# Kernel tuning notes

Hardware: AMD Instinct MI355X
Metric: run time of the kernel (lower is better)

## Reference

```python
import jax, jax.numpy as jnp
import numpy as np

B, S = 32, 2048
D = 128      # embedding_dim
H = 256      # hidden_dim
K = 512      # codebook_size
RECON_COEF, COMMIT_COEF, VQ_COEF = 1.0, 0.15, 0.05


def _conv1d(x, w, b):
    # x: [B, Cin, S], w: [Cout, Cin, 3], 'SAME' padding (padding=1, k=3)
    y = jax.lax.conv_general_dilated(x, w, window_strides=(1,), padding='SAME',
                                     dimension_numbers=('NCH', 'OIH', 'NCH'))
    return y + b[None, :, None]


def _lrelu(x):
    return jnp.where(x >= 0, x, 0.2 * x)


def setup_inputs() -> dict:
    key = jax.random.key(0)
    ks = jax.random.split(key, 14)

    def w(k, shape, fan_in):
        bound = 1.0 / np.sqrt(fan_in)
        return jax.random.uniform(k, shape, jnp.float32, -bound, bound)

    return {
        'x': jax.random.normal(ks[0], (B, S), jnp.float32),
        'codebook': jax.random.normal(ks[1], (K, D), jnp.float32),
        'ew1': w(ks[2], (H, 1, 3), 1 * 3),  'eb1': w(ks[3], (H,), 1 * 3),
        'ew2': w(ks[4], (H, H, 3), H * 3),  'eb2': w(ks[5], (H,), H * 3),
        'ew3': w(ks[6], (D, H, 3), H * 3),  'eb3': w(ks[7], (D,), H * 3),
        'dw1': w(ks[8], (H, D, 3), D * 3),  'db1': w(ks[9], (H,), D * 3),
        'dw2': w(ks[10], (H, H, 3), H * 3), 'db2': w(ks[11], (H,), H * 3),
        'dw3': w(ks[12], (1, H, 3), H * 3), 'db3': w(ks[13], (1,), H * 3),
    }


def reference(x, codebook, ew1, eb1, ew2, eb2, ew3, eb3, dw1, db1, dw2, db2, dw3, db3):
    # ---- encode ----
    h = x[:, None, :]                                  # [B,1,S]
    h = _lrelu(_conv1d(h, ew1, eb1))
    h = _lrelu(_conv1d(h, ew2, eb2))
    z = _conv1d(h, ew3, eb3)                           # [B,D,S]

    # ---- vector quantize (eval mode: no EMA update) ----
    zt = jnp.transpose(z, (0, 2, 1))                   # [B,S,D]
    z_flat = zt.reshape(-1, D)                         # [B*S,D]
    # squared distances: |z|^2 + |c|^2 - 2 z c^T
    d = (jnp.sum(z_flat ** 2, axis=1, keepdims=True)
         + jnp.sum(codebook ** 2, axis=1)
         - 2.0 * z_flat @ codebook.T)                  # [B*S,K]
    idx = jnp.argmin(d, axis=1)                        # [B*S]
    z_q = codebook[idx].reshape(zt.shape)              # [B,S,D] (== one-hot @ codebook)

    vq_loss = jnp.mean((jax.lax.stop_gradient(zt) - z_q) ** 2) * VQ_COEF
    commitment_loss = jnp.mean((zt - jax.lax.stop_gradient(z_q)) ** 2) * COMMIT_COEF
    indices = idx.reshape(B, S)

    # ---- decode ----
    h = jnp.transpose(z_q, (0, 2, 1))                  # [B,D,S]
    h = _lrelu(_conv1d(h, dw1, db1))
    h = _lrelu(_conv1d(h, dw2, db2))
    x_recon = _conv1d(h, dw3, db3)[:, 0, :]            # [B,S]

    recon_loss = jnp.mean((x - x_recon) ** 2) * RECON_COEF
    loss = recon_loss + vq_loss + commitment_loss
    return x_recon, indices, loss, recon_loss, vq_loss, commitment_loss
```

## Files before the change

kernel.cpp:

```cpp
#include <hip/hip_runtime.h>
#include <float.h>

#define S_LEN 2048
#define BATCH 32
#define HCH   256
#define DCH   128
#define KCODES 512

typedef float  f32x4  __attribute__((ext_vector_type(4)));
typedef short  bf16x8 __attribute__((ext_vector_type(8)));
typedef short  short8 __attribute__((ext_vector_type(8)));

__device__ __forceinline__ float lrelu_f(float v) { return v >= 0.f ? v : 0.2f * v; }

__device__ __forceinline__ short f2bf(float f) {
    unsigned u = __float_as_uint(f);
    u = u + 0x7fffu + ((u >> 16) & 1u);
    return (short)(u >> 16);
}
__device__ __forceinline__ float bf2f(unsigned short u) {
    return __uint_as_float(((unsigned)u) << 16);
}

__global__ void prep_cb_split_kernel(const float* __restrict__ cb,
                                     short* __restrict__ cb_hi, short* __restrict__ cb_lo,
                                     float* __restrict__ cnorm) {
    int k = blockIdx.x * 256 + threadIdx.x;
    if (k < KCODES) {
        float s = 0.f;
        for (int d = 0; d < DCH; ++d) {
            float v = cb[k * DCH + d];
            s += v * v;
            short hi = f2bf(v);
            short lo = f2bf(v - bf2f((unsigned short)hi));
            cb_hi[k * DCH + d] = hi;
            cb_lo[k * DCH + d] = lo;
        }
        cnorm[k] = s;
    }
}

__global__ void prep_w_split_kernel(const float* __restrict__ Wsrc,
                                    short* __restrict__ Wh, short* __restrict__ Wl,
                                    int Cout, int Cin) {
    int i = blockIdx.x * 256 + threadIdx.x;
    int total = 3 * Cout * Cin;
    if (i < total) {
        int t = i / (Cout * Cin);
        int rem = i - t * Cout * Cin;
        int co = rem / Cin;
        int ci = rem - co * Cin;
        float v = Wsrc[(co * Cin + ci) * 3 + t];
        short hi = f2bf(v);
        Wh[i] = hi;
        Wl[i] = f2bf(v - bf2f((unsigned short)hi));
    }
}

__global__ void prep_wdec_kernel(const float* __restrict__ Wsrc, short* __restrict__ Wdst,
                                 int Cin) {
    int i = blockIdx.x * 256 + threadIdx.x;
    int total = 3 * 256 * Cin;
    if (i < total) {
        int t = i / (256 * Cin);
        int rem = i - t * 256 * Cin;
        int co = rem / Cin;
        int ci = rem - co * Cin;
        Wdst[i] = f2bf(Wsrc[(co * Cin + ci) * 3 + t]);
    }
}

__global__ void prep_w3t_kernel(const float* __restrict__ w3, float* __restrict__ w3t) {
    int i = blockIdx.x * 256 + threadIdx.x;
    if (i < 768) {
        int t = i / 256, ci = i - t * 256;
        w3t[i] = w3[ci * 3 + t];
    }
}

__global__ __launch_bounds__(256) void enc_conv1_cl_kernel(
        const float* __restrict__ x, short* __restrict__ h_hi, short* __restrict__ h_lo,
        const float* __restrict__ w, const float* __restrict__ bias) {
    __shared__ float ws[HCH * 3];
    __shared__ float bs[HCH];
    int tid = threadIdx.x;
    for (int i = tid; i < HCH * 3; i += 256) ws[i] = w[i];
    for (int i = tid; i < HCH; i += 256) bs[i] = bias[i];
    __syncthreads();
    int b = blockIdx.y;
    int s = blockIdx.x * 32 + (tid >> 3);
    int cch = tid & 7;
    const float* xb = x + (size_t)b * S_LEN;
    float xm = (s > 0) ? xb[s - 1] : 0.f;
    float x0 = xb[s];
    float xp = (s < S_LEN - 1) ? xb[s + 1] : 0.f;
    size_t base = ((size_t)(b * S_LEN + s)) * HCH + cch * 32;
#pragma unroll
    for (int cc = 0; cc < 4; ++cc) {
        short8 oh, ol;
#pragma unroll
        for (int e = 0; e < 8; ++e) {
            int co = cch * 32 + cc * 8 + e;
            float v = ws[co * 3 + 0] * xm + ws[co * 3 + 1] * x0 + ws[co * 3 + 2] * xp + bs[co];
            v = lrelu_f(v);
            short hi = f2bf(v);
            oh[e] = hi;
            ol[e] = f2bf(v - bf2f((unsigned short)hi));
        }
        *(short8*)(h_hi + base + cc * 8) = oh;
        *(short8*)(h_lo + base + cc * 8) = ol;
    }
}

__global__ __launch_bounds__(256) void conv_mfma_split(
        const short* __restrict__ in_hi, const short* __restrict__ in_lo,
        short* __restrict__ out_hi, short* __restrict__ out_lo,
        const short* __restrict__ wt_hi, const short* __restrict__ wt_lo,
        const float* __restrict__ bias, int Cin, int Cout, int do_lrelu) {
    __shared__ short smem[17680];
    short* Xh = smem;
    short* Xl = smem + 130 * 68;

    const int tid = threadIdx.x;
    const int lane = tid & 63;
    const int w = tid >> 6;
    const int m = lane & 15;
    const int q = lane >> 4;
    const int sOff = (w & 1) * 64;
    const int cOff = (w >> 1) * 64;
    const int b = blockIdx.z;
    const int s0 = blockIdx.x * 128;
    const int co0 = blockIdx.y * 128;

    f32x4 acc[4][4];
    f32x4 zero4 = {0.f, 0.f, 0.f, 0.f};
#pragma unroll
    for (int i = 0; i < 4; ++i)
#pragma unroll
        for (int j = 0; j < 4; ++j) acc[i][j] = zero4;

    const short* inhb = in_hi + (size_t)b * S_LEN * Cin;
    const short* inlb = in_lo + (size_t)b * S_LEN * Cin;

    for (int ci0 = 0; ci0 < Cin; ci0 += 64) {
        __syncthreads();
        for (int c = tid; c < 2080; c += 256) {
            int r = c >> 4;
            int sub = c & 15;
            int half = sub >> 3;
            int part = sub & 7;
            int s = s0 - 1 + r;
            float4 v = make_float4(0.f, 0.f, 0.f, 0.f);
            if (s >= 0 && s < S_LEN) {
                size_t goff = (size_t)s * Cin + ci0 + part * 8;
                v = half ? *(const float4*)(inlb + goff) : *(const float4*)(inhb + goff);
            }
            *(float4*)((half ? Xl : Xh) + r * 68 + part * 8) = v;
        }
        __syncthreads();

#pragma unroll
        for (int ks = 0; ks < 2; ++ks) {
            const int kofs = ks * 32;
#pragma unroll
            for (int t = 0; t < 3; ++t) {
                bf16x8 ah[4], al[4], bh[4], bl[4];
#pragma unroll
                for (int j = 0; j < 4; ++j) {
                    size_t woff = ((size_t)(t * Cout + co0 + cOff + j * 16 + m)) * Cin + ci0 + kofs + q * 8;
                    bh[j] = *(const bf16x8*)(wt_hi + woff);
                    bl[j] = *(const bf16x8*)(wt_lo + woff);
                }
#pragma unroll
                for (int i = 0; i < 4; ++i) {
                    int row = sOff + i * 16 + m + t;
                    ah[i] = *(const bf16x8*)(Xh + row * 68 + kofs + q * 8);
                    al[i] = *(const bf16x8*)(Xl + row * 68 + kofs + q * 8);
                }
#pragma unroll
                for (int i = 0; i < 4; ++i)
#pragma unroll
                    for (int j = 0; j < 4; ++j) {
                        acc[i][j] = __builtin_amdgcn_mfma_f32_16x16x32_bf16(ah[i], bh[j], acc[i][j], 0, 0, 0);
                        acc[i][j] = __builtin_amdgcn_mfma_f32_16x16x32_bf16(ah[i], bl[j], acc[i][j], 0, 0, 0);
                        acc[i][j] = __builtin_amdgcn_mfma_f32_16x16x32_bf16(al[i], bh[j], acc[i][j], 0, 0, 0);
                    }
            }
        }
    }

    __syncthreads();
    short* obH = smem + w * 2560;
    short* obL = obH + 1280;
#pragma unroll
    for (int j = 0; j < 4; ++j) {
        float bv = bias[co0 + cOff + j * 16 + m];
#pragma unroll
        for (int i = 0; i < 4; ++i) {
#pragma unroll
            for (int r = 0; r < 4; ++r) {
                float val = acc[i][j][r] + bv;
                if (do_lrelu) val = lrelu_f(val);
                short hi = f2bf(val);
                short lo = f2bf(val - bf2f((unsigned short)hi));
                int row = i * 16 + q * 4 + r;
                obH[row * 20 + m] = hi;
                obL[row * 20 + m] = lo;
            }
        }
        const int colchunk = lane & 1;
        const int rbase = lane >> 1;
#pragma unroll
        for (int it = 0; it < 2; ++it) {
            int row = it * 32 + rbase;
            short8 vh = *(const short8*)(obH + row * 20 + colchunk * 8);
            short8 vl = *(const short8*)(obL + row * 20 + colchunk * 8);
            size_t goff = ((size_t)(b * S_LEN + s0 + sOff + row)) * Cout
                        + co0 + cOff + j * 16 + colchunk * 8;
            *(short8*)(out_hi + goff) = vh;
            *(short8*)(out_lo + goff) = vl;
        }
    }
}

__global__ __launch_bounds__(256) void vq_mfma_kernel(
        const short* __restrict__ z_hi, const short* __restrict__ z_lo,
        const short* __restrict__ cb_hi, const short* __restrict__ cb_lo,
        const float* __restrict__ cnorm, int* __restrict__ idx_out,
        float* __restrict__ idx_f_out) {
    __shared__ short smem[2 * 64 * 136];
    __shared__ float redv[64][4];
    __shared__ int   redi[64][4];
    short* Zh = smem;
    short* Zl = smem + 64 * 136;

    const int tid = threadIdx.x;
    const int lane = tid & 63;
    const int w = tid >> 6;
    const int m = lane & 15;
    const int q = lane >> 4;
    const int n0 = blockIdx.x * 64;

    for (int c = tid; c < 2048; c += 256) {
        int buf = c >> 10;
        int rem = c & 1023;
        int r = rem >> 4, part = rem & 15;
        size_t goff = (size_t)(n0 + r) * DCH + part * 8;
        float4 v = buf ? *(const float4*)(z_lo + goff) : *(const float4*)(z_hi + goff);
        *(float4*)((buf ? Zl : Zh) + r * 136 + part * 8) = v;
    }
    __syncthreads();

    float best[4][4];
    int besti[4][4];
#pragma unroll
    for (int i = 0; i < 4; ++i)
#pragma unroll
        for (int r = 0; r < 4; ++r) { best[i][r] = FLT_MAX; besti[i][r] = 0; }

    for (int k0 = 0; k0 < KCODES; k0 += 256) {
        f32x4 acc[4][4];
        f32x4 zero4 = {0.f, 0.f, 0.f, 0.f};
#pragma unroll
        for (int i = 0; i < 4; ++i)
#pragma unroll
            for (int j = 0; j < 4; ++j) acc[i][j] = zero4;

#pragma unroll
        for (int d0 = 0; d0 < DCH; d0 += 32) {
            bf16x8 ah[4], al[4], bh[4], bl[4];
#pragma unroll
            for (int j = 0; j < 4; ++j) {
                size_t coff = (size_t)(k0 + w * 64 + j * 16 + m) * DCH + d0 + q * 8;
                bh[j] = *(const bf16x8*)(cb_hi + coff);
                bl[j] = *(const bf16x8*)(cb_lo + coff);
            }
#pragma unroll
            for (int i = 0; i < 4; ++i) {
                int row = i * 16 + m;
                ah[i] = *(const bf16x8*)(Zh + row * 136 + d0 + q * 8);
                al[i] = *(const bf16x8*)(Zl + row * 136 + d0 + q * 8);
            }
#pragma unroll
            for (int i = 0; i < 4; ++i)
#pragma unroll
                for (int j = 0; j < 4; ++j) {
                    acc[i][j] = __builtin_amdgcn_mfma_f32_16x16x32_bf16(ah[i], bh[j], acc[i][j], 0, 0, 0);
                    acc[i][j] = __builtin_amdgcn_mfma_f32_16x16x32_bf16(ah[i], bl[j], acc[i][j], 0, 0, 0);
                    acc[i][j] = __builtin_amdgcn_mfma_f32_16x16x32_bf16(al[i], bh[j], acc[i][j], 0, 0, 0);
                }
        }
#pragma unroll
        for (int j = 0; j < 4; ++j) {
            int k = k0 + w * 64 + j * 16 + m;
            float cn = cnorm[k];
#pragma unroll
            for (int i = 0; i < 4; ++i)
#pragma unroll
                for (int r = 0; r < 4; ++r) {
                    float dv = cn - 2.f * acc[i][j][r];
                    if (dv < best[i][r]) { best[i][r] = dv; besti[i][r] = k; }
                }
        }
    }

#pragma unroll
    for (int mask = 1; mask < 16; mask <<= 1) {
#pragma unroll
        for (int i = 0; i < 4; ++i)
#pragma unroll
            for (int r = 0; r < 4; ++r) {
                float ov = __shfl_xor(best[i][r], mask);
                int oi = __shfl_xor(besti[i][r], mask);
                if (ov < best[i][r] || (ov == best[i][r] && oi < besti[i][r])) {
                    best[i][r] = ov; besti[i][r] = oi;
                }
            }
    }
    if (m == 0) {
#pragma unroll
        for (int i = 0; i < 4; ++i)
#pragma unroll
            for (int r = 0; r < 4; ++r) {
                int srow = i * 16 + q * 4 + r;
                redv[srow][w] = best[i][r];
                redi[srow][w] = besti[i][r];
            }
    }
    __syncthreads();
    if (tid < 64) {
        float bv = redv[tid][0];
        int bi = redi[tid][0];
#pragma unroll
        for (int w2 = 1; w2 < 4; ++w2) {
            float v = redv[tid][w2];
            int ii = redi[tid][w2];
            if (v < bv || (v == bv && ii < bi)) { bv = v; bi = ii; }
        }
        int n = n0 + tid;
        idx_out[n] = bi;
        idx_f_out[n] = (float)bi;
    }
}

__global__ __launch_bounds__(256) void gather_vqsum_kernel(
        const float* __restrict__ cb, const int* __restrict__ idxb,
        const short* __restrict__ z_hi, const short* __restrict__ z_lo,
        short* __restrict__ zq, float* __restrict__ acc_vq) {
    int tid = threadIdx.x;
    int b = blockIdx.y;
    int s = blockIdx.x * 32 + (tid >> 3);
    int dpart = tid & 7;
    int n = b * S_LEN + s;
    int k = idxb[n];
    const float* src = cb + (size_t)k * DCH + dpart * 16;
    size_t zoff = (size_t)n * DCH + dpart * 16;
    float sum = 0.f;
    short8 outv[2];
#pragma unroll
    for (int half = 0; half < 2; ++half) {
        float4 f0 = *(const float4*)(src + half * 8);
        float4 f1 = *(const float4*)(src + half * 8 + 4);
        bf16x8 zh = *(const bf16x8*)(z_hi + zoff + half * 8);
        bf16x8 zl = *(const bf16x8*)(z_lo + zoff + half * 8);
        float qv[8] = {f0.x, f0.y, f0.z, f0.w, f1.x, f1.y, f1.z, f1.w};
        short8 o;
#pragma unroll
        for (int e = 0; e < 8; ++e) {
            o[e] = f2bf(qv[e]);
            float zv = bf2f((unsigned short)zh[e]) + bf2f((unsigned short)zl[e]);
            float df = zv - qv[e];
            sum += df * df;
        }
        outv[half] = o;
    }
    *(short8*)(zq + zoff) = outv[0];
    *(short8*)(zq + zoff + 8) = outv[1];
    for (int off = 32; off > 0; off >>= 1) sum += __shfl_down(sum, off);
    __shared__ float wsum[4];
    if ((tid & 63) == 0) wsum[tid >> 6] = sum;
    __syncthreads();
    if (tid == 0) atomicAdd(acc_vq, wsum[0] + wsum[1] + wsum[2] + wsum[3]);
}

__global__ __launch_bounds__(256) void conv_mfma_cl(
        const short* __restrict__ in, short* __restrict__ out,
        const short* __restrict__ wt, const float* __restrict__ bias,
        int Cin) {
    __shared__ short smem[8840];
    short* Xs = smem;

    const int tid = threadIdx.x;
    const int lane = tid & 63;
    const int w = tid >> 6;
    const int m = lane & 15;
    const int q = lane >> 4;
    const int sOff = (w & 1) * 64;
    const int cOff = (w >> 1) * 64;
    const int b = blockIdx.z;
    const int s0 = blockIdx.x * 128;
    const int co0 = blockIdx.y * 128;

    f32x4 acc[4][4];
    f32x4 zero4 = {0.f, 0.f, 0.f, 0.f};
#pragma unroll
    for (int i = 0; i < 4; ++i)
#pragma unroll
        for (int j = 0; j < 4; ++j) acc[i][j] = zero4;

    const short* inb = in + (size_t)b * S_LEN * Cin;

    for (int ci0 = 0; ci0 < Cin; ci0 += 64) {
        __syncthreads();
        for (int c = tid; c < 1040; c += 256) {
            int r = c >> 3;
            int part = c & 7;
            int s = s0 - 1 + r;
            float4 v = make_float4(0.f, 0.f, 0.f, 0.f);
            if (s >= 0 && s < S_LEN)
                v = *(const float4*)(inb + (size_t)s * Cin + ci0 + part * 8);
            *(float4*)(Xs + r * 68 + part * 8) = v;
        }
        __syncthreads();

#pragma unroll
        for (int ks = 0; ks < 2; ++ks) {
            const int kofs = ks * 32;
#pragma unroll
            for (int t = 0; t < 3; ++t) {
                bf16x8 a[4], bb[4];
#pragma unroll
                for (int j = 0; j < 4; ++j)
                    bb[j] = *(const bf16x8*)(wt + ((size_t)(t * 256 + co0 + cOff + j * 16 + m)) * Cin + ci0 + kofs + q * 8);
#pragma unroll
                for (int i = 0; i < 4; ++i)
                    a[i] = *(const bf16x8*)(Xs + (sOff + i * 16 + m + t) * 68 + kofs + q * 8);
#pragma unroll
                for (int i = 0; i < 4; ++i)
#pragma unroll
                    for (int j = 0; j < 4; ++j)
                        acc[i][j] = __builtin_amdgcn_mfma_f32_16x16x32_bf16(
                            a[i], bb[j], acc[i][j], 0, 0, 0);
            }
        }
    }

    __syncthreads();
    short* ob = smem + w * 1280;
#pragma unroll
    for (int j = 0; j < 4; ++j) {
        float bv = bias[co0 + cOff + j * 16 + m];
#pragma unroll
        for (int i = 0; i < 4; ++i) {
#pragma unroll
            for (int r = 0; r < 4; ++r) {
                float val = acc[i][j][r] + bv;
                val = lrelu_f(val);
                ob[(i * 16 + q * 4 + r) * 20 + m] = f2bf(val);
            }
        }
        const int colchunk = lane & 1;
        const int rbase = lane >> 1;
#pragma unroll
        for (int it = 0; it < 2; ++it) {
            int row = it * 32 + rbase;
            short8 v = *(const short8*)(ob + row * 20 + colchunk * 8);
            size_t goff = ((size_t)(b * S_LEN + s0 + sOff + row)) * 256
                        + co0 + cOff + j * 16 + colchunk * 8;
            *(short8*)(out + goff) = v;
        }
    }
}

__global__ __launch_bounds__(256) void dec_conv3_tiled_kernel(
        const short* __restrict__ h, const float* __restrict__ w3t,
        const float* __restrict__ b3, const float* __restrict__ x,
        float* __restrict__ xr, float* __restrict__ acc_recon) {
    __shared__ short Zs[66 * 264];
    __shared__ float ws[3 * 256];
    __shared__ float wsum[4];
    int tid = threadIdx.x;
    int b = blockIdx.y;
    int s0 = blockIdx.x * 64;
    const short* hb = h + (size_t)b * S_LEN * HCH;
    for (int i = tid; i < 768; i += 256) ws[i] = w3t[i];
    for (int c = tid; c < 2112; c += 256) {
        int r = c >> 5, part = c & 31;
        int g = s0 - 1 + r;
        short8 v = {0, 0, 0, 0, 0, 0, 0, 0};
        if (g >= 0 && g < S_LEN)
            v = *(const short8*)(hb + (size_t)g * HCH + part * 8);
        *(short8*)(Zs + r * 264 + part * 8) = v;
    }
    __syncthreads();

    int quarter = tid & 3;
    int sl = tid >> 2;
    float a0 = 0.f, a1 = 0.f, a2 = 0.f, a3 = 0.f;
#pragma unroll
    for (int t = 0; t < 3; ++t) {
        const short* zrow = Zs + (sl + t) * 264 + quarter * 64;
        const float* wrow = ws + t * 256 + quarter * 64;
#pragma unroll
        for (int c = 0; c < 8; ++c) {
            bf16x8 v = *(const bf16x8*)(zrow + c * 8);
            float4 w0 = *(const float4*)(wrow + c * 8);
            float4 w1 = *(const float4*)(wrow + c * 8 + 4);
            a0 = fmaf(w0.x, bf2f((unsigned short)v[0]), a0);
            a1 = fmaf(w0.y, bf2f((unsigned short)v[1]), a1);
            a2 = fmaf(w0.z, bf2f((unsigned short)v[2]), a2);
            a3 = fmaf(w0.w, bf2f((unsigned short)v[3]), a3);
            a0 = fmaf(w1.x, bf2f((unsigned short)v[4]), a0);
            a1 = fmaf(w1.y, bf2f((unsigned short)v[5]), a1);
            a2 = fmaf(w1.z, bf2f((unsigned short)v[6]), a2);
            a3 = fmaf(w1.w, bf2f((unsigned short)v[7]), a3);
        }
    }
    float acc = (a0 + a1) + (a2 + a3);
    acc += __shfl_xor(acc, 1);
    acc += __shfl_xor(acc, 2);
    float df2 = 0.f;
    if (quarter == 0) {
        int s = s0 + sl;
        float tot = acc + b3[0];
        xr[b * S_LEN + s] = tot;
        float df = x[b * S_LEN + s] - tot;
        df2 = df * df;
    }
    for (int off = 32; off > 0; off >>= 1) df2 += __shfl_down(df2, off);
    int lane = tid & 63, wv = tid >> 6;
    if (lane == 0) wsum[wv] = df2;
    __syncthreads();
    if (tid == 0) atomicAdd(acc_recon, wsum[0] + wsum[1] + wsum[2] + wsum[3]);
}

__global__ void finalize_kernel(const float* __restrict__ accs, float* __restrict__ out) {
    if (threadIdx.x == 0) {
        float vqm = accs[0] / ((float)BATCH * S_LEN * DCH);
        float rm  = accs[1] / ((float)BATCH * S_LEN);
        float vq_loss = vqm * 0.05f;
        float commit  = vqm * 0.15f;
        float recon   = rm * 1.0f;
        out[0] = recon + vq_loss + commit;
        out[1] = recon;
        out[2] = vq_loss;
        out[3] = commit;
    }
}

extern "C" void kernel_launch(void* const* d_in, const int* in_sizes, int n_in,
                              void* d_out, int out_size, void* d_ws, size_t ws_size,
                              hipStream_t stream) {
    const float* x    = (const float*)d_in[0];
    const float* cb   = (const float*)d_in[1];
    const float* ew1  = (const float*)d_in[2];
    const float* eb1  = (const float*)d_in[3];
    const float* ew2  = (const float*)d_in[4];
    const float* eb2  = (const float*)d_in[5];
    const float* ew3  = (const float*)d_in[6];
    const float* eb3  = (const float*)d_in[7];
    const float* dw1  = (const float*)d_in[8];
    const float* db1  = (const float*)d_in[9];
    const float* dw2  = (const float*)d_in[10];
    const float* db2  = (const float*)d_in[11];
    const float* dw3  = (const float*)d_in[12];
    const float* db3  = (const float*)d_in[13];

    float* out = (float*)d_out;
    float* xr    = out;
    float* idx_f = out + BATCH * S_LEN;
    float* loss_out = out + 2 * BATCH * S_LEN;

    const size_t NH = (size_t)BATCH * S_LEN * HCH;
    const size_t ND = (size_t)BATCH * S_LEN * DCH;

    short* sp = (short*)d_ws;
    short* h1_hi = sp;
    short* h1_lo = sp + NH;
    short* z_hi  = sp;
    short* z_lo  = sp + ND;
    short* h1d_bf = sp;
    short* h2_hi = sp + 2 * NH;
    short* h2_lo = sp + 3 * NH;
    short* zq_bf = sp + 2 * NH;
    short* h2d_bf = sp + 3 * NH;
    short* sm = sp + 4 * NH;
    short* cb_hi = sm; sm += KCODES * DCH;
    short* cb_lo = sm; sm += KCODES * DCH;
    short* w2_hi = sm; sm += 3 * HCH * HCH;
    short* w2_lo = sm; sm += 3 * HCH * HCH;
    short* w3_hi = sm; sm += 3 * DCH * HCH;
    short* w3_lo = sm; sm += 3 * DCH * HCH;
    short* wbf_d1 = sm; sm += 3 * 256 * DCH;
    short* wbf_d2 = sm; sm += 3 * 256 * HCH;
    float* cnorm = (float*)sm;
    int* idxb = (int*)(cnorm + KCODES);
    float* w3t = (float*)(idxb + BATCH * S_LEN);
    float* accs = w3t + 768;

    hipMemsetAsync(accs, 0, 2 * sizeof(float), stream);

    prep_cb_split_kernel<<<2, 256, 0, stream>>>(cb, cb_hi, cb_lo, cnorm);
    prep_w_split_kernel<<<(3 * HCH * HCH + 255) / 256, 256, 0, stream>>>(ew2, w2_hi, w2_lo, HCH, HCH);
    prep_w_split_kernel<<<(3 * DCH * HCH + 255) / 256, 256, 0, stream>>>(ew3, w3_hi, w3_lo, DCH, HCH);
    prep_wdec_kernel<<<(3 * 256 * DCH + 255) / 256, 256, 0, stream>>>(dw1, wbf_d1, DCH);
    prep_wdec_kernel<<<(3 * 256 * HCH + 255) / 256, 256, 0, stream>>>(dw2, wbf_d2, HCH);
    prep_w3t_kernel<<<3, 256, 0, stream>>>(dw3, w3t);

    enc_conv1_cl_kernel<<<dim3(S_LEN / 32, BATCH), 256, 0, stream>>>(x, h1_hi, h1_lo, ew1, eb1);
    conv_mfma_split<<<dim3(S_LEN / 128, HCH / 128, BATCH), 256, 0, stream>>>(
        h1_hi, h1_lo, h2_hi, h2_lo, w2_hi, w2_lo, eb2, HCH, HCH, 1);
    conv_mfma_split<<<dim3(S_LEN / 128, DCH / 128, BATCH), 256, 0, stream>>>(
        h2_hi, h2_lo, z_hi, z_lo, w3_hi, w3_lo, eb3, HCH, DCH, 0);

    vq_mfma_kernel<<<(BATCH * S_LEN) / 64, 256, 0, stream>>>(
        z_hi, z_lo, cb_hi, cb_lo, cnorm, idxb, idx_f);
    gather_vqsum_kernel<<<dim3(S_LEN / 32, BATCH), 256, 0, stream>>>(
        cb, idxb, z_hi, z_lo, zq_bf, accs);

    conv_mfma_cl<<<dim3(S_LEN / 128, 2, BATCH), 256, 0, stream>>>(
        zq_bf, h1d_bf, wbf_d1, db1, DCH);
    conv_mfma_cl<<<dim3(S_LEN / 128, 2, BATCH), 256, 0, stream>>>(
        h1d_bf, h2d_bf, wbf_d2, db2, HCH);
    dec_conv3_tiled_kernel<<<dim3(S_LEN / 64, BATCH), 256, 0, stream>>>(
        h2d_bf, w3t, db3, x, xr, accs + 1);

    finalize_kernel<<<1, 64, 0, stream>>>(accs, loss_out);
}
```

Baseline: 569.2 us.

## Double-buffer input tiles with register prefetch in encoder and decoder MFMA convs

Both MFMA conv kernels now stage input tiles through two LDS buffers with a 32-channel K chunk. The next chunk is prefetched into registers before the current chunk's MFMAs, then written into the other buffer, so each iteration needs one barrier instead of two. This is meant to hide global load latency behind MFMA work. It costs more LDS, extra prefetch registers, and twice as many loop iterations because the chunks are smaller.

```diff
diff --git a/kernel.cpp b/kernel.cpp
--- a/kernel.cpp
+++ b/kernel.cpp
@@ -117,9 +117,7 @@
         short* __restrict__ out_hi, short* __restrict__ out_lo,
         const short* __restrict__ wt_hi, const short* __restrict__ wt_lo,
         const float* __restrict__ bias, int Cin, int Cout, int do_lrelu) {
-    __shared__ short smem[17680];
-    short* Xh = smem;
-    short* Xl = smem + 130 * 68;
+    __shared__ short smem[20800];
 
     const int tid = threadIdx.x;
     const int lane = tid & 63;
@@ -139,53 +137,76 @@
 #pragma unroll
         for (int j = 0; j < 4; ++j) acc[i][j] = zero4;
 
-    const short* inhb = in_hi + (size_t)b * S_LEN * Cin;
-    const short* inlb = in_lo + (size_t)b * S_LEN * Cin;
-
-    for (int ci0 = 0; ci0 < Cin; ci0 += 64) {
-        __syncthreads();
-        for (int c = tid; c < 2080; c += 256) {
-            int r = c >> 4;
-            int sub = c & 15;
-            int half = sub >> 3;
-            int part = sub & 7;
-            int s = s0 - 1 + r;
-            float4 v = make_float4(0.f, 0.f, 0.f, 0.f);
-            if (s >= 0 && s < S_LEN) {
-                size_t goff = (size_t)s * Cin + ci0 + part * 8;
-                v = half ? *(const float4*)(inlb + goff) : *(const float4*)(inhb + goff);
-            }
-            *(float4*)((half ? Xl : Xh) + r * 68 + part * 8) = v;
-        }
-        __syncthreads();
-
-#pragma unroll
-        for (int ks = 0; ks < 2; ++ks) {
-            const int kofs = ks * 32;
-#pragma unroll
-            for (int t = 0; t < 3; ++t) {
-                bf16x8 ah[4], al[4], bh[4], bl[4];
+    const int half = (tid >> 2) & 1;
+    const int p8 = (tid & 3) * 8;
+    const int srow = tid >> 3;
+    const short* gsrc = half ? (in_lo + (size_t)b * S_LEN * Cin)
+                             : (in_hi + (size_t)b * S_LEN * Cin);
+    const short* gptr = gsrc + (size_t)(s0 + srow) * Cin + p8;
+    const int hs = (tid >> 3) ? (s0 + 128) : (s0 - 1);
+    const bool hvalid = (tid < 16) && hs >= 0 && hs < S_LEN;
+    const short* hptr = gsrc + (size_t)(hvalid ? hs : 0) * Cin + p8;
+    const int hrow = (tid >> 3) ? 129 : 0;
+    const size_t cstride = (size_t)32 * Cin;
+
+    float4 pf0, pf1, pf2, pf3, ph;
+
+#define ENC_PREFETCH(CI0) do {                                              \
+    pf0 = *(const float4*)(gptr + (CI0));                                   \
+    pf1 = *(const float4*)(gptr + cstride + (CI0));                         \
+    pf2 = *(const float4*)(gptr + 2 * cstride + (CI0));                     \
+    pf3 = *(const float4*)(gptr + 3 * cstride + (CI0));                     \
+    ph = make_float4(0.f, 0.f, 0.f, 0.f);                                   \
+    if (hvalid) ph = *(const float4*)(hptr + (CI0)); } while (0)
+
+#define ENC_WRITEBUF(BUF) do {                                              \
+    short* dst = smem + (BUF) * 10400 + half * 5200 + (srow + 1) * 40 + p8; \
+    *(float4*)dst = pf0;                                                    \
+    *(float4*)(dst + 32 * 40) = pf1;                                        \
+    *(float4*)(dst + 64 * 40) = pf2;                                        \
+    *(float4*)(dst + 96 * 40) = pf3;                                        \
+    if (tid < 16)                                                           \
+        *(float4*)(smem + (BUF) * 10400 + half * 5200 + hrow * 40 + p8) = ph; } while (0)
+
+    const int NC = Cin >> 5;
+
+    ENC_PREFETCH(0);
+    ENC_WRITEBUF(0);
+    __syncthreads();
+    if (NC > 1) ENC_PREFETCH(32);
+
+    for (int c = 0; c < NC; ++c) {
+        const short* Xh = smem + (c & 1) * 10400;
+        const short* Xl = Xh + 5200;
+        const int ci0 = c * 32;
+#pragma unroll
+        for (int t = 0; t < 3; ++t) {
+            bf16x8 ah[4], al[4], bh[4], bl[4];
+#pragma unroll
+            for (int j = 0; j < 4; ++j) {
+                size_t woff = ((size_t)(t * Cout + co0 + cOff + j * 16 + m)) * Cin + ci0 + q * 8;
+                bh[j] = *(const bf16x8*)(wt_hi + woff);
+                bl[j] = *(const bf16x8*)(wt_lo + woff);
+            }
+#pragma unroll
+            for (int i = 0; i < 4; ++i) {
+                int row = sOff + i * 16 + m + t;
+                ah[i] = *(const bf16x8*)(Xh + row * 40 + q * 8);
+                al[i] = *(const bf16x8*)(Xl + row * 40 + q * 8);
+            }
+#pragma unroll
+            for (int i = 0; i < 4; ++i)
 #pragma unroll
                 for (int j = 0; j < 4; ++j) {
-                    size_t woff = ((size_t)(t * Cout + co0 + cOff + j * 16 + m)) * Cin + ci0 + kofs + q * 8;
-                    bh[j] = *(const bf16x8*)(wt_hi + woff);
-                    bl[j] = *(const bf16x8*)(wt_lo + woff);
+                    acc[i][j] = __builtin_amdgcn_mfma_f32_16x16x32_bf16(ah[i], bh[j], acc[i][j], 0, 0, 0);
+                    acc[i][j] = __builtin_amdgcn_mfma_f32_16x16x32_bf16(ah[i], bl[j], acc[i][j], 0, 0, 0);
+                    acc[i][j] = __builtin_amdgcn_mfma_f32_16x16x32_bf16(al[i], bh[j], acc[i][j], 0, 0, 0);
                 }
-#pragma unroll
-                for (int i = 0; i < 4; ++i) {
-                    int row = sOff + i * 16 + m + t;
-                    ah[i] = *(const bf16x8*)(Xh + row * 68 + kofs + q * 8);
-                    al[i] = *(const bf16x8*)(Xl + row * 68 + kofs + q * 8);
-                }
-#pragma unroll
-                for (int i = 0; i < 4; ++i)
-#pragma unroll
-                    for (int j = 0; j < 4; ++j) {
-                        acc[i][j] = __builtin_amdgcn_mfma_f32_16x16x32_bf16(ah[i], bh[j], acc[i][j], 0, 0, 0);
-                        acc[i][j] = __builtin_amdgcn_mfma_f32_16x16x32_bf16(ah[i], bl[j], acc[i][j], 0, 0, 0);
-                        acc[i][j] = __builtin_amdgcn_mfma_f32_16x16x32_bf16(al[i], bh[j], acc[i][j], 0, 0, 0);
-                    }
-            }
+        }
+        if (c + 1 < NC) {
+            ENC_WRITEBUF((c + 1) & 1);
+            __syncthreads();
+            if (c + 2 < NC) ENC_PREFETCH((c + 2) * 32);
         }
     }
 
@@ -221,6 +242,8 @@
             *(short8*)(out_lo + goff) = vl;
         }
     }
+#undef ENC_PREFETCH
+#undef ENC_WRITEBUF
 }
 
 __global__ __launch_bounds__(256) void vq_mfma_kernel(
@@ -387,8 +410,7 @@
         const short* __restrict__ in, short* __restrict__ out,
         const short* __restrict__ wt, const float* __restrict__ bias,
         int Cin) {
-    __shared__ short smem[8840];
-    short* Xs = smem;
+    __shared__ short smem[10400];
 
     const int tid = threadIdx.x;
     const int lane = tid & 63;
@@ -408,40 +430,61 @@
 #pragma unroll
         for (int j = 0; j < 4; ++j) acc[i][j] = zero4;
 
-    const short* inb = in + (size_t)b * S_LEN * Cin;
-
-    for (int ci0 = 0; ci0 < Cin; ci0 += 64) {
-        __syncthreads();
-        for (int c = tid; c < 1040; c += 256) {
-            int r = c >> 3;
-            int part = c & 7;
-            int s = s0 - 1 + r;
-            float4 v = make_float4(0.f, 0.f, 0.f, 0.f);
-            if (s >= 0 && s < S_LEN)
-                v = *(const float4*)(inb + (size_t)s * Cin + ci0 + part * 8);
-            *(float4*)(Xs + r * 68 + part * 8) = v;
-        }
-        __syncthreads();
-
-#pragma unroll
-        for (int ks = 0; ks < 2; ++ks) {
-            const int kofs = ks * 32;
-#pragma unroll
-            for (int t = 0; t < 3; ++t) {
-                bf16x8 a[4], bb[4];
+    const int p8 = (tid & 3) * 8;
+    const int srow = tid >> 2;
+    const short* gsrc = in + (size_t)b * S_LEN * Cin;
+    const short* gptr = gsrc + (size_t)(s0 + srow) * Cin + p8;
+    const int hs = (tid >> 2) ? (s0 + 128) : (s0 - 1);
+    const bool hvalid = (tid < 8) && hs >= 0 && hs < S_LEN;
+    const short* hptr = gsrc + (size_t)(hvalid ? hs : 0) * Cin + p8;
+    const int hrow = (tid >> 2) ? 129 : 0;
+    const size_t cstride = (size_t)64 * Cin;
+
+    float4 pf0, pf1, ph;
+
+#define DEC_PREFETCH(CI0) do {                                              \
+    pf0 = *(const float4*)(gptr + (CI0));                                   \
+    pf1 = *(const float4*)(gptr + cstride + (CI0));                         \
+    ph = make_float4(0.f, 0.f, 0.f, 0.f);                                   \
+    if (hvalid) ph = *(const float4*)(hptr + (CI0)); } while (0)
+
+#define DEC_WRITEBUF(BUF) do {                                              \
+    short* dst = smem + (BUF) * 5200 + (srow + 1) * 40 + p8;                \
+    *(float4*)dst = pf0;                                                    \
+    *(float4*)(dst + 64 * 40) = pf1;                                        \
+    if (tid < 8)                                                            \
+        *(float4*)(smem + (BUF) * 5200 + hrow * 40 + p8) = ph; } while (0)
+
+    const int NC = Cin >> 5;
+
+    DEC_PREFETCH(0);
+    DEC_WRITEBUF(0);
+    __syncthreads();
+    if (NC > 1) DEC_PREFETCH(32);
+
+    for (int c = 0; c < NC; ++c) {
+        const short* Xs = smem + (c & 1) * 5200;
+        const int ci0 = c * 32;
+#pragma unroll
+        for (int t = 0; t < 3; ++t) {
+            bf16x8 a[4], bb[4];
+#pragma unroll
+            for (int j = 0; j < 4; ++j)
+                bb[j] = *(const bf16x8*)(wt + ((size_t)(t * 256 + co0 + cOff + j * 16 + m)) * Cin + ci0 + q * 8);
+#pragma unroll
+            for (int i = 0; i < 4; ++i)
+                a[i] = *(const bf16x8*)(Xs + (sOff + i * 16 + m + t) * 40 + q * 8);
+#pragma unroll
+            for (int i = 0; i < 4; ++i)
 #pragma unroll
                 for (int j = 0; j < 4; ++j)
-                    bb[j] = *(const bf16x8*)(wt + ((size_t)(t * 256 + co0 + cOff + j * 16 + m)) * Cin + ci0 + kofs + q * 8);
-#pragma unroll
-                for (int i = 0; i < 4; ++i)
-                    a[i] = *(const bf16x8*)(Xs + (sOff + i * 16 + m + t) * 68 + kofs + q * 8);
-#pragma unroll
-                for (int i = 0; i < 4; ++i)
-#pragma unroll
-                    for (int j = 0; j < 4; ++j)
-                        acc[i][j] = __builtin_amdgcn_mfma_f32_16x16x32_bf16(
-                            a[i], bb[j], acc[i][j], 0, 0, 0);
-            }
+                    acc[i][j] = __builtin_amdgcn_mfma_f32_16x16x32_bf16(
+                        a[i], bb[j], acc[i][j], 0, 0, 0);
+        }
+        if (c + 1 < NC) {
+            DEC_WRITEBUF((c + 1) & 1);
+            __syncthreads();
+            if (c + 2 < NC) DEC_PREFETCH((c + 2) * 32);
         }
     }
 
@@ -470,6 +513,8 @@
             *(short8*)(out + goff) = v;
         }
     }
+#undef DEC_PREFETCH
+#undef DEC_WRITEBUF
 }
 
 __global__ __launch_bounds__(256) void dec_conv3_tiled_kernel(
```

Measured after the change: 527.6 us. -7.3%, faster.
